# Kernel tuning notes

Measured on AMD Instinct MI355X. Metric: run time of the kernel, lower is better.

## Reference

```python
import jax, jax.numpy as jnp
import numpy as np

NUM_LAYERS = 2
FEATURES = 128
INPUT_SIZE = 128
HIDDEN = 512
BATCH = 128
SEQ_LEN = 512
PRED_LEN = 128


def _uniform(key, shape, fan):
    bound = 1.0 / np.sqrt(fan)
    return jax.random.uniform(key, shape, jnp.float32, -bound, bound)


def setup_inputs() -> dict:
    key = jax.random.key(0)
    ks = jax.random.split(key, 14)
    inp = {}
    inp["x"] = jax.random.normal(ks[0], (BATCH, SEQ_LEN, FEATURES), jnp.float32)
    # encoder Linear(features -> input_size)
    inp["enc_w"] = _uniform(ks[1], (INPUT_SIZE, FEATURES), FEATURES)
    inp["enc_b"] = _uniform(ks[2], (INPUT_SIZE,), FEATURES)
    # decoder Linear(hidden -> input_size)
    inp["dec_w"] = _uniform(ks[3], (INPUT_SIZE, HIDDEN), HIDDEN)
    inp["dec_b"] = _uniform(ks[4], (INPUT_SIZE,), HIDDEN)
    # LSTM layer 0 (input_size -> hidden), gate order i,f,g,o as in PyTorch
    inp["wih0"] = _uniform(ks[5], (4 * HIDDEN, INPUT_SIZE), HIDDEN)
    inp["whh0"] = _uniform(ks[6], (4 * HIDDEN, HIDDEN), HIDDEN)
    inp["bih0"] = _uniform(ks[7], (4 * HIDDEN,), HIDDEN)
    inp["bhh0"] = _uniform(ks[8], (4 * HIDDEN,), HIDDEN)
    # LSTM layer 1 (hidden -> hidden)
    inp["wih1"] = _uniform(ks[9], (4 * HIDDEN, HIDDEN), HIDDEN)
    inp["whh1"] = _uniform(ks[10], (4 * HIDDEN, HIDDEN), HIDDEN)
    inp["bih1"] = _uniform(ks[11], (4 * HIDDEN,), HIDDEN)
    inp["bhh1"] = _uniform(ks[12], (4 * HIDDEN,), HIDDEN)
    inp["pred_len"] = PRED_LEN
    return inp


def _lstm_cell(h, c, inp, wih, whh, bih, bhh):
    g = inp @ wih.T + bih + h @ whh.T + bhh  # [B, 4H]
    i, f, gg, o = jnp.split(g, 4, axis=-1)
    c = jax.nn.sigmoid(f) * c + jax.nn.sigmoid(i) * jnp.tanh(gg)
    h = jax.nn.sigmoid(o) * jnp.tanh(c)
    return h, c


def reference(x, enc_w, enc_b, dec_w, dec_b, wih0, whh0, bih0, bhh0,
              wih1, whh1, bih1, bhh1, pred_len):
    B, S, Fdim = x.shape
    T = S + pred_len - 1
    # pad x to T steps; beyond S the input comes from the previous output
    x_pad = jnp.concatenate([x, jnp.zeros((B, pred_len - 1, Fdim), x.dtype)], axis=1)
    x_t = jnp.transpose(x_pad, (1, 0, 2))  # [T, B, F]

    def step(carry, xs):
        h0, c0, h1, c1, prev_out = carry
        xt, t = xs
        inp = jnp.where(t < S, xt, prev_out)
        e = inp @ enc_w.T + enc_b                    # encoder
        h0, c0 = _lstm_cell(h0, c0, e, wih0, whh0, bih0, bhh0)
        h1, c1 = _lstm_cell(h1, c1, h0, wih1, whh1, bih1, bhh1)
        out = h1 @ dec_w.T + dec_b                   # decoder
        return (h0, c0, h1, c1, out), out

    z = jnp.zeros((B, HIDDEN), x.dtype)
    init = (z, z, z, z, jnp.zeros((B, Fdim), x.dtype))
    _, outs = jax.lax.scan(step, init, (x_t, jnp.arange(T)))
    # keep steps idx >= S-1 (pred_len outputs), back to [B, pred_len, input_size]
    return jnp.transpose(outs[S - 1:], (1, 0, 2))
```

## Files before the change

kernel.cpp:

```cpp
#include <hip/hip_runtime.h>
#include <math.h>

#define HID 512
#define FEAT 128
#define SEQL 512
#define PREDL 128
#define NWG 256
#define R0 648
#define R1 520

__device__ __forceinline__ float sigf_(float x) { return 1.0f / (1.0f + __expf(-x)); }
__device__ __forceinline__ float tanh_(float x) {
  float ax = fabsf(x);
  float e2 = __expf(-2.0f * ax);
  return copysignf((1.0f - e2) / (1.0f + e2), x);
}
__device__ __forceinline__ void stg_sc(float* p, float v) {
  __hip_atomic_store(p, v, __ATOMIC_RELAXED, __HIP_MEMORY_SCOPE_AGENT);
}

__device__ __forceinline__ void bar_arr(int* __restrict__ bar, int grp,
                                        int slot, int phase, int tid) {
  __syncthreads();
  if (tid == 0)
    __hip_atomic_store(bar + grp * 8 + slot, phase, __ATOMIC_RELAXED,
                       __HIP_MEMORY_SCOPE_AGENT);
  asm volatile("" ::: "memory");
}
__device__ __forceinline__ void bar_wai(int* __restrict__ bar, int grp,
                                        int phase, int tid,
                                        int* __restrict__ ldsph) {
  asm volatile("" ::: "memory");
  if (tid < 64) {
    for (;;) {
      int v = phase;
      if (tid < 8)
        v = __hip_atomic_load(bar + grp * 8 + tid, __ATOMIC_RELAXED,
                              __HIP_MEMORY_SCOPE_AGENT);
      if (__ballot(v >= phase) == 0xFFFFFFFFFFFFFFFFULL) break;
      __builtin_amdgcn_s_sleep(1);
    }
    if (tid == 0)
      __hip_atomic_store(ldsph, phase, __ATOMIC_RELAXED,
                         __HIP_MEMORY_SCOPE_WORKGROUP);
  } else {
    float z = 1.0f;
    while (__hip_atomic_load(ldsph, __ATOMIC_RELAXED,
                             __HIP_MEMORY_SCOPE_WORKGROUP) < phase) {
#pragma unroll
      for (int i = 0; i < 64; ++i) z = __builtin_fmaf(z, 1.0000001f, 1.0e-9f);
      asm volatile("" : "+v"(z));
    }
  }
  __syncthreads();
}

__device__ __forceinline__ void load1(const float4* p, float4& r) {
  asm volatile("global_load_dwordx4 %0, %1, off sc0 sc1\n\ts_waitcnt vmcnt(0)"
               : "=&v"(r) : "v"(p) : "memory");
}
__device__ __forceinline__ void issue1(const float4* p, float4& r) {
  asm volatile("global_load_dwordx4 %0, %1, off sc0 sc1"
               : "=&v"(r) : "v"(p) : "memory");
}

__global__ __launch_bounds__(1024, 1) void k_teacher(
    const float* __restrict__ x, const float* __restrict__ ENCW,
    const float* __restrict__ enc_b,
    const float* __restrict__ W0T, const float* __restrict__ W1F,
    const float* __restrict__ bih0, const float* __restrict__ bhh0,
    const float* __restrict__ bih1, const float* __restrict__ bhh1,
    float* __restrict__ h0A, float* __restrict__ h0B,
    float* __restrict__ h1A, float* __restrict__ h1B,
    float* __restrict__ cbuf, int* __restrict__ bar) {
  __shared__ float h0l[4 * R0];
  __shared__ float h1l[4 * R0];
  __shared__ float xl[4 * 132];
  __shared__ float sg0[1024];
  __shared__ float sg1[1024];
  __shared__ int lds_ph;

  const int wg = blockIdx.x, tid = threadIdx.x;
  const int grp = wg >> 3, slot = wg & 7;
  const int b = tid & 3, ul = (tid >> 2) & 63, g = tid >> 8;
  const int n = g * 512 + slot * 64 + ul;
  const int rowoff = n;

  float* h0b[2] = {h0A, h0B};
  float* h1b[2] = {h1A, h1B};
  const float4* W0 = (const float4*)W0T + rowoff;
  const float4* W1 = (const float4*)W1F + rowoff;
  const float4* E4 = (const float4*)ENCW;

  const float bt0 = bih0[n] + bhh0[n];
  const float b1f = bih1[n] + bhh1[n];

  const int ldh0 = (tid < 512);
  const int lu = tid & 511;
  const int fe = (tid >> 2) & 127, be = tid & 3;
  const float encb = enc_b[fe];

  const float* h0row = h0l + b * R0;
  const float* h1row = h1l + b * R0;

  float c_reg = 0.0f;
  int ph = 0;
  if (tid == 0) lds_ph = 0;
  if (tid < 128) {
    const int bx = tid >> 5, f4 = tid & 31;
    *(float4*)(xl + bx * 132 + f4 * 4) =
        *(const float4*)(x + ((size_t)(grp * 4 + bx) * SEQL + 0) * FEAT + f4 * 4);
  }
  __syncthreads();

  for (int t = 0; t < SEQL; ++t) {
    const float* src = (ldh0 ? h0b[(t + 1) & 1] : h1b[t & 1]) + grp * 2048;
    const float4* sp = (const float4*)src + lu;
    float4 r;
    issue1(sp, r);

    if (tid < 512) {
      float e = encb;
#pragma unroll 8
      for (int k4 = 0; k4 < 32; ++k4) {
        const float4 w = E4[k4 * 128 + fe];
        const float4 xv = *(const float4*)(xl + be * 132 + k4 * 4);
        e += w.x * xv.x + w.y * xv.y + w.z * xv.z + w.w * xv.w;
      }
      h0l[be * R0 + 512 + fe] = e;
    }
    asm volatile("s_waitcnt vmcnt(0)" ::: "memory");
    float* dl = ldh0 ? h0l : h1l;
    dl[0 * R0 + lu] = r.x; dl[1 * R0 + lu] = r.y;
    dl[2 * R0 + lu] = r.z; dl[3 * R0 + lu] = r.w;
    __syncthreads();

    float a0 = bt0, a0b = 0.f;
#pragma unroll 4
    for (int k4 = 0; k4 < 160; ++k4) {
      const float4 w = W0[(size_t)k4 * 2048];
      const float4 h = *(const float4*)(h0row + k4 * 4);
      a0 = __builtin_fmaf(w.x, h.x, a0);
      a0b = __builtin_fmaf(w.y, h.y, a0b);
      a0 = __builtin_fmaf(w.z, h.z, a0);
      a0b = __builtin_fmaf(w.w, h.w, a0b);
    }
    a0 += a0b;
    float a1 = b1f, a1b = 0.f;
#pragma unroll 4
    for (int k4 = 0; k4 < 128; ++k4) {
      const float4 w = W1[(size_t)k4 * 2048];
      const float4 h = *(const float4*)(h0row + k4 * 4);
      a1 = __builtin_fmaf(w.x, h.x, a1);
      a1b = __builtin_fmaf(w.y, h.y, a1b);
      a1 = __builtin_fmaf(w.z, h.z, a1);
      a1b = __builtin_fmaf(w.w, h.w, a1b);
    }
#pragma unroll 4
    for (int k4 = 0; k4 < 128; ++k4) {
      const float4 w = W1[(size_t)(128 + k4) * 2048];
      const float4 h = *(const float4*)(h1row + k4 * 4);
      a1 = __builtin_fmaf(w.x, h.x, a1);
      a1b = __builtin_fmaf(w.y, h.y, a1b);
      a1 = __builtin_fmaf(w.z, h.z, a1);
      a1b = __builtin_fmaf(w.w, h.w, a1b);
    }
    a1 += a1b;
    sg0[tid] = a0;
    sg1[tid] = a1;
    __syncthreads();

    if (tid < 256) {
      const float ig = sigf_(sg0[tid]), fg = sigf_(sg0[256 + tid]);
      const float gg = tanh_(sg0[512 + tid]), og = sigf_(sg0[768 + tid]);
      const float cn = fg * c_reg + ig * gg;
      c_reg = cn;
      stg_sc(h0b[t & 1] + grp * 2048 + slot * 256 + tid, og * tanh_(cn));
    } else if (tid < 512 && t > 0) {
      const int l = tid - 256;
      const float ig = sigf_(sg1[l]), fg = sigf_(sg1[256 + l]);
      const float gg = tanh_(sg1[512 + l]), og = sigf_(sg1[768 + l]);
      const float cn = fg * c_reg + ig * gg;
      c_reg = cn;
      stg_sc(h1b[(t + 1) & 1] + grp * 2048 + slot * 256 + l, og * tanh_(cn));
    }
    bar_arr(bar, grp, slot, ++ph, tid);
    if (tid < 128 && t + 1 < SEQL) {
      const int bx = tid >> 5, f4 = tid & 31;
      *(float4*)(xl + bx * 132 + f4 * 4) =
          *(const float4*)(x + ((size_t)(grp * 4 + bx) * SEQL + (t + 1)) * FEAT + f4 * 4);
    }
    bar_wai(bar, grp, ph, tid, &lds_ph);
  }

  if (tid < 256) cbuf[(size_t)wg * 256 + tid] = c_reg;
  else if (tid < 512) cbuf[65536 + (size_t)wg * 256 + (tid - 256)] = c_reg;
}

__global__ __launch_bounds__(1024, 1) void k_ar(
    const float* __restrict__ WAF, const float* __restrict__ W1F,
    const float* __restrict__ DECW, const float* __restrict__ dec_b,
    const float* __restrict__ bih0, const float* __restrict__ bhh0,
    const float* __restrict__ bih1, const float* __restrict__ bhh1,
    const float* __restrict__ bcomp,
    float* __restrict__ h0A, float* __restrict__ h0B,
    float* __restrict__ h1A, float* __restrict__ h1B,
    float* __restrict__ cbuf, int* __restrict__ bar,
    float* __restrict__ out) {
  __shared__ float hAl[4 * R1];
  __shared__ float hBl[4 * R1];
  __shared__ float sg0[1024];
  __shared__ float sg1[1024];
  __shared__ float sdec[256];
  __shared__ int lds_ph;

  const int wg = blockIdx.x, tid = threadIdx.x;
  const int grp = wg >> 3, slot = wg & 7;
  const int b = tid & 3, ul = (tid >> 2) & 63, g = tid >> 8;
  const int n = g * 512 + slot * 64 + ul;

  float* h0b[2] = {h0A, h0B};
  float* h1b[2] = {h1A, h1B};
  const float4* WA = (const float4*)WAF + n;
  const float4* W1 = (const float4*)W1F + n;
  const float4* D4 = (const float4*)DECW;

  const float baf = bih0[n] + bhh0[n] + bcomp[n];
  const float b1f = bih1[n] + bhh1[n];

  const int lu = tid & 511;
  const float* hArow = hAl + b * R1;
  const float* hBrow = hBl + b * R1;

  const int d = tid - 512;
  const int dfl = d & 15, dbb = (d >> 4) & 3, dq = (d >> 6) & 3;
  const int fdec = slot * 16 + dfl;
  const float decb = dec_b[fdec & 127];

  float c_reg = 0.0f;
  if (tid < 256) c_reg = cbuf[(size_t)wg * 256 + tid];
  else if (tid < 512) c_reg = cbuf[65536 + (size_t)wg * 256 + (tid - 256)];

  int ph = 0;
  if (tid == 0) lds_ph = 0;
  __syncthreads();

  {
    const float* src = (tid < 512 ? h0b[1] : h1b[0]) + grp * 2048;
    float4 r;
    load1((const float4*)src + lu, r);
    float* dl = (tid < 512) ? hBl : hAl;
    dl[0 * R1 + lu] = r.x; dl[1 * R1 + lu] = r.y;
    dl[2 * R1 + lu] = r.z; dl[3 * R1 + lu] = r.w;
    __syncthreads();
    float a1 = b1f, a1b = 0.f;
#pragma unroll 4
    for (int k4 = 0; k4 < 128; ++k4) {
      const float4 w = W1[(size_t)k4 * 2048];
      const float4 h = *(const float4*)(hBrow + k4 * 4);
      a1 = __builtin_fmaf(w.x, h.x, a1);  a1b = __builtin_fmaf(w.y, h.y, a1b);
      a1 = __builtin_fmaf(w.z, h.z, a1);  a1b = __builtin_fmaf(w.w, h.w, a1b);
    }
#pragma unroll 4
    for (int k4 = 0; k4 < 128; ++k4) {
      const float4 w = W1[(size_t)(128 + k4) * 2048];
      const float4 h = *(const float4*)(hArow + k4 * 4);
      a1 = __builtin_fmaf(w.x, h.x, a1);  a1b = __builtin_fmaf(w.y, h.y, a1b);
      a1 = __builtin_fmaf(w.z, h.z, a1);  a1b = __builtin_fmaf(w.w, h.w, a1b);
    }
    sg1[tid] = a1 + a1b;
    __syncthreads();
    if (tid >= 256 && tid < 512) {
      const int l = tid - 256;
      const float ig = sigf_(sg1[l]), fg = sigf_(sg1[256 + l]);
      const float gg = tanh_(sg1[512 + l]), og = sigf_(sg1[768 + l]);
      const float cn = fg * c_reg + ig * gg;
      c_reg = cn;
      stg_sc(h1b[1] + grp * 2048 + slot * 256 + l, og * tanh_(cn));
    }
    bar_arr(bar, grp, slot, ++ph, tid);
    bar_wai(bar, grp, ph, tid, &lds_ph);
  }

  for (int t = SEQL; t < SEQL + PREDL - 1; ++t) {
    {
      const float* src = (tid < 512 ? h1b[(t + 1) & 1] : h0b[(t + 1) & 1]) + grp * 2048;
      float4 r;
      load1((const float4*)src + lu, r);
      float* dl = (tid < 512) ? hAl : hBl;
      dl[0 * R1 + lu] = r.x; dl[1 * R1 + lu] = r.y;
      dl[2 * R1 + lu] = r.z; dl[3 * R1 + lu] = r.w;
      __syncthreads();
      float aA = baf, aAb = 0.f;
#pragma unroll 4
      for (int k4 = 0; k4 < 128; ++k4) {
        const float4 w = WA[(size_t)k4 * 2048];
        const float4 h = *(const float4*)(hArow + k4 * 4);
        aA = __builtin_fmaf(w.x, h.x, aA);  aAb = __builtin_fmaf(w.y, h.y, aAb);
        aA = __builtin_fmaf(w.z, h.z, aA);  aAb = __builtin_fmaf(w.w, h.w, aAb);
      }
#pragma unroll 4
      for (int k4 = 0; k4 < 128; ++k4) {
        const float4 w = WA[(size_t)(128 + k4) * 2048];
        const float4 h = *(const float4*)(hBrow + k4 * 4);
        aA = __builtin_fmaf(w.x, h.x, aA);  aAb = __builtin_fmaf(w.y, h.y, aAb);
        aA = __builtin_fmaf(w.z, h.z, aA);  aAb = __builtin_fmaf(w.w, h.w, aAb);
      }
      sg0[tid] = aA + aAb;
      if (tid >= 512 && tid < 768) {
        float p = 0.f;
        const float* hr = hAl + dbb * R1;
#pragma unroll 4
        for (int k4 = dq * 32; k4 < dq * 32 + 32; ++k4) {
          const float4 w = D4[k4 * 128 + fdec];
          const float4 h = *(const float4*)(hr + k4 * 4);
          p += w.x * h.x + w.y * h.y + w.z * h.z + w.w * h.w;
        }
        sdec[d] = p;
      }
      __syncthreads();
      if (tid < 256) {
        const float ig = sigf_(sg0[tid]), fg = sigf_(sg0[256 + tid]);
        const float gg = tanh_(sg0[512 + tid]), og = sigf_(sg0[768 + tid]);
        const float cn = fg * c_reg + ig * gg;
        c_reg = cn;
        stg_sc(h0b[t & 1] + grp * 2048 + slot * 256 + tid, og * tanh_(cn));
      }
      if (tid >= 512 && tid < 576) {
        const float s = decb + sdec[d] + sdec[d + 64] + sdec[d + 128] + sdec[d + 192];
        out[((size_t)(grp * 4 + dbb) * PREDL + (t - SEQL)) * FEAT + fdec] = s;
      }
      bar_arr(bar, grp, slot, ++ph, tid);
      bar_wai(bar, grp, ph, tid, &lds_ph);
    }
    {
      if (tid < 512) {
        const float* src = h0b[t & 1] + grp * 2048;
        float4 r;
        load1((const float4*)src + lu, r);
        hBl[0 * R1 + lu] = r.x; hBl[1 * R1 + lu] = r.y;
        hBl[2 * R1 + lu] = r.z; hBl[3 * R1 + lu] = r.w;
      }
      __syncthreads();
      float a1 = b1f, a1b = 0.f;
#pragma unroll 4
      for (int k4 = 0; k4 < 128; ++k4) {
        const float4 w = W1[(size_t)k4 * 2048];
        const float4 h = *(const float4*)(hBrow + k4 * 4);
        a1 = __builtin_fmaf(w.x, h.x, a1);  a1b = __builtin_fmaf(w.y, h.y, a1b);
        a1 = __builtin_fmaf(w.z, h.z, a1);  a1b = __builtin_fmaf(w.w, h.w, a1b);
      }
#pragma unroll 4
      for (int k4 = 0; k4 < 128; ++k4) {
        const float4 w = W1[(size_t)(128 + k4) * 2048];
        const float4 h = *(const float4*)(hArow + k4 * 4);
        a1 = __builtin_fmaf(w.x, h.x, a1);  a1b = __builtin_fmaf(w.y, h.y, a1b);
        a1 = __builtin_fmaf(w.z, h.z, a1);  a1b = __builtin_fmaf(w.w, h.w, a1b);
      }
      sg1[tid] = a1 + a1b;
      __syncthreads();
      if (tid >= 256 && tid < 512) {
        const int l = tid - 256;
        const float ig = sigf_(sg1[l]), fg = sigf_(sg1[256 + l]);
        const float gg = tanh_(sg1[512 + l]), og = sigf_(sg1[768 + l]);
        const float cn = fg * c_reg + ig * gg;
        c_reg = cn;
        stg_sc(h1b[t & 1] + grp * 2048 + slot * 256 + l, og * tanh_(cn));
      }
      bar_arr(bar, grp, slot, ++ph, tid);
      bar_wai(bar, grp, ph, tid, &lds_ph);
    }
  }

  {
    if (tid < 512) {
      const float* src = h1b[0] + grp * 2048;
      float4 r;
      load1((const float4*)src + lu, r);
      hAl[0 * R1 + lu] = r.x; hAl[1 * R1 + lu] = r.y;
      hAl[2 * R1 + lu] = r.z; hAl[3 * R1 + lu] = r.w;
    }
    __syncthreads();
    if (tid >= 512 && tid < 768) {
      float p = 0.f;
      const float* hr = hAl + dbb * R1;
#pragma unroll 4
      for (int k4 = dq * 32; k4 < dq * 32 + 32; ++k4) {
        const float4 w = D4[k4 * 128 + fdec];
        const float4 h = *(const float4*)(hr + k4 * 4);
        p += w.x * h.x + w.y * h.y + w.z * h.z + w.w * h.w;
      }
      sdec[d] = p;
    }
    __syncthreads();
    if (tid >= 512 && tid < 576) {
      const float s = decb + sdec[d] + sdec[d + 64] + sdec[d + 128] + sdec[d + 192];
      out[((size_t)(grp * 4 + dbb) * PREDL + (PREDL - 1)) * FEAT + fdec] = s;
    }
  }
}

__global__ void k_b1(const float* __restrict__ enc_w,
                     const float* __restrict__ dec_w, float* __restrict__ B1) {
  const int idx = blockIdx.x * 256 + threadIdx.x;
  const int j = idx >> 9, m = idx & 511;
  float acc = 0.0f;
  for (int k = 0; k < FEAT; ++k) acc += enc_w[j * FEAT + k] * dec_w[k * HID + m];
  B1[idx] = acc;
}
__global__ void k_te(const float* __restrict__ enc_w,
                     const float* __restrict__ enc_b,
                     const float* __restrict__ dec_b, float* __restrict__ te) {
  const int j = threadIdx.x;
  float acc = enc_b[j];
  for (int k = 0; k < FEAT; ++k) acc += dec_b[k] * enc_w[j * FEAT + k];
  te[j] = acc;
}
__global__ void k_bcomp(const float* __restrict__ wih0,
                        const float* __restrict__ te, float* __restrict__ bc) {
  const int nn = blockIdx.x * 256 + threadIdx.x;
  float acc = 0.0f;
  for (int j = 0; j < FEAT; ++j) acc += wih0[nn * FEAT + j] * te[j];
  bc[nn] = acc;
}
__global__ void k_w0t(const float* __restrict__ whh0,
                      const float* __restrict__ wih0, float* __restrict__ W) {
  const int idx = blockIdx.x * 256 + threadIdx.x;
  const int k4 = idx >> 11, rr = idx & 2047;
  const int k = k4 * 4;
  float4 v;
  if (k < 512) {
    const float* p = whh0 + (size_t)rr * 512 + k;
    v = make_float4(p[0], p[1], p[2], p[3]);
  } else {
    const float* p = wih0 + (size_t)rr * 128 + (k - 512);
    v = make_float4(p[0], p[1], p[2], p[3]);
  }
  ((float4*)W)[idx] = v;
}
__global__ void k_w1f(const float* __restrict__ wih1,
                      const float* __restrict__ whh1, float* __restrict__ W) {
  const int idx = blockIdx.x * 256 + threadIdx.x;
  const int k4 = idx >> 11, rr = idx & 2047;
  const int k = k4 * 4;
  const float* p = (k < 512) ? (wih1 + (size_t)rr * 512 + k)
                             : (whh1 + (size_t)rr * 512 + (k - 512));
  ((float4*)W)[idx] = make_float4(p[0], p[1], p[2], p[3]);
}
__global__ void k_waf(const float* __restrict__ wih0,
                      const float* __restrict__ B1,
                      const float* __restrict__ whh0, float* __restrict__ W) {
  const int idx = blockIdx.x * 256 + threadIdx.x;
  const int k4 = idx >> 11, rr = idx & 2047;
  const int k = k4 * 4;
  float4 v;
  if (k < 512) {
    float s0 = 0, s1 = 0, s2 = 0, s3 = 0;
    const float* wr = wih0 + (size_t)rr * 128;
    for (int j = 0; j < 128; ++j) {
      const float wv = wr[j];
      const float* bp = B1 + (size_t)j * 512 + k;
      s0 += wv * bp[0]; s1 += wv * bp[1]; s2 += wv * bp[2]; s3 += wv * bp[3];
    }
    v = make_float4(s0, s1, s2, s3);
  } else {
    const float* p = whh0 + (size_t)rr * 512 + (k - 512);
    v = make_float4(p[0], p[1], p[2], p[3]);
  }
  ((float4*)W)[idx] = v;
}
__global__ void k_encw(const float* __restrict__ enc_w, float* __restrict__ W) {
  const int idx = blockIdx.x * 256 + threadIdx.x;
  const int k4 = idx >> 7, f = idx & 127;
  const float* p = enc_w + (size_t)f * 128 + k4 * 4;
  ((float4*)W)[idx] = make_float4(p[0], p[1], p[2], p[3]);
}
__global__ void k_decw(const float* __restrict__ dec_w, float* __restrict__ W) {
  const int idx = blockIdx.x * 256 + threadIdx.x;
  const int k4 = idx >> 7, f = idx & 127;
  const float* p = dec_w + (size_t)f * 512 + k4 * 4;
  ((float4*)W)[idx] = make_float4(p[0], p[1], p[2], p[3]);
}

#define WS_H0A 0
#define WS_H0B 65536
#define WS_H1A 131072
#define WS_H1B 196608
#define WS_CBUF 262144
#define WS_BART 393216
#define WS_BARA 397312
#define WS_TE 401408
#define WS_BCOMP 401536
#define WS_B1 403584
#define WS_ENCW 469120
#define WS_DECW 485504
#define WS_W0T 551040
#define WS_W1F 1861760
#define WS_WAF 3958912

extern "C" void kernel_launch(void* const* d_in, const int* in_sizes, int n_in,
                              void* d_out, int out_size, void* d_ws,
                              size_t ws_size, hipStream_t stream) {
  const float* x     = (const float*)d_in[0];
  const float* enc_w = (const float*)d_in[1];
  const float* enc_b = (const float*)d_in[2];
  const float* dec_w = (const float*)d_in[3];
  const float* dec_b = (const float*)d_in[4];
  const float* wih0  = (const float*)d_in[5];
  const float* whh0  = (const float*)d_in[6];
  const float* bih0  = (const float*)d_in[7];
  const float* bhh0  = (const float*)d_in[8];
  const float* wih1  = (const float*)d_in[9];
  const float* whh1  = (const float*)d_in[10];
  const float* bih1  = (const float*)d_in[11];
  const float* bhh1  = (const float*)d_in[12];
  float* out = (float*)d_out;

  float* ws = (float*)d_ws;
  float* h0A = ws + WS_H0A;
  float* h0B = ws + WS_H0B;
  float* h1A = ws + WS_H1A;
  float* h1B = ws + WS_H1B;
  float* cbuf = ws + WS_CBUF;
  int* barT = (int*)(ws + WS_BART);
  int* barA = (int*)(ws + WS_BARA);
  float* te = ws + WS_TE;
  float* bcomp = ws + WS_BCOMP;
  float* B1 = ws + WS_B1;
  float* ENCW = ws + WS_ENCW;
  float* DECW = ws + WS_DECW;
  float* W0T = ws + WS_W0T;
  float* W1F = ws + WS_W1F;
  float* WAF = ws + WS_WAF;

  (void)hipMemsetAsync(ws, 0, (size_t)262144 * sizeof(float), stream);
  (void)hipMemsetAsync(ws + WS_BART, 0, (size_t)8192 * sizeof(float), stream);

  k_b1<<<256, 256, 0, stream>>>(enc_w, dec_w, B1);
  k_te<<<1, 128, 0, stream>>>(enc_w, enc_b, dec_b, te);
  k_bcomp<<<8, 256, 0, stream>>>(wih0, te, bcomp);
  k_w0t<<<1280, 256, 0, stream>>>(whh0, wih0, W0T);
  k_w1f<<<2048, 256, 0, stream>>>(wih1, whh1, W1F);
  k_waf<<<2048, 256, 0, stream>>>(wih0, B1, whh0, WAF);
  k_encw<<<16, 256, 0, stream>>>(enc_w, ENCW);
  k_decw<<<64, 256, 0, stream>>>(dec_w, DECW);

  k_teacher<<<NWG, 1024, 0, stream>>>(
      x, ENCW, enc_b, W0T, W1F, bih0, bhh0, bih1, bhh1,
      h0A, h0B, h1A, h1B, cbuf, barT);

  k_ar<<<NWG, 1024, 0, stream>>>(
      WAF, W1F, DECW, dec_b, bih0, bhh0, bih1, bhh1, bcomp,
      h0A, h0B, h1A, h1B, cbuf, barA, out);
}
```

Before: 37.98 ms.

## Split teacher phase into per-layer producer/consumer workgroups linked by a ring buffer

Replaces the 256-workgroup teacher kernel, which needed an 8-workgroup global barrier every step, with 64 workgroups. Each batch group of 4 gets one workgroup for layer 0 and one for layer 1, each owning all 2048 gate rows, so the recurrent state stays in LDS. Layer 0 publishes h0 into an 8-deep ring in global memory guarded by producer/consumer counters, which lets the two layers run pipelined instead of in lockstep. The cost is far less parallelism: 64 workgroups instead of 256, each thread computing 8 gate rows per step and streaming the whole weight matrix through one CU.

After: 126.0 ms. 232% more time.

```diff
diff --git a/kernel.cpp b/kernel.cpp
--- a/kernel.cpp
+++ b/kernel.cpp
@@ -8,6 +8,7 @@
 #define NWG 256
 #define R0 648
 #define R1 520
+#define RD 8
 
 __device__ __forceinline__ float sigf_(float x) { return 1.0f / (1.0f + __expf(-x)); }
 __device__ __forceinline__ float tanh_(float x) {
@@ -54,147 +55,218 @@
   }
   __syncthreads();
 }
-
 __device__ __forceinline__ void load1(const float4* p, float4& r) {
   asm volatile("global_load_dwordx4 %0, %1, off sc0 sc1\n\ts_waitcnt vmcnt(0)"
                : "=&v"(r) : "v"(p) : "memory");
 }
-__device__ __forceinline__ void issue1(const float4* p, float4& r) {
-  asm volatile("global_load_dwordx4 %0, %1, off sc0 sc1"
-               : "=&v"(r) : "v"(p) : "memory");
-}
-
-__global__ __launch_bounds__(1024, 1) void k_teacher(
+
+__global__ __launch_bounds__(1024, 1) void k_rails(
     const float* __restrict__ x, const float* __restrict__ ENCW,
     const float* __restrict__ enc_b,
     const float* __restrict__ W0T, const float* __restrict__ W1F,
     const float* __restrict__ bih0, const float* __restrict__ bhh0,
     const float* __restrict__ bih1, const float* __restrict__ bhh1,
-    float* __restrict__ h0A, float* __restrict__ h0B,
-    float* __restrict__ h1A, float* __restrict__ h1B,
-    float* __restrict__ cbuf, int* __restrict__ bar) {
+    float* __restrict__ h0fin,
+    float* __restrict__ h1fin,
+    float* __restrict__ ring, int* __restrict__ pctr, int* __restrict__ cctr,
+    float* __restrict__ cbuf) {
   __shared__ float h0l[4 * R0];
-  __shared__ float h1l[4 * R0];
   __shared__ float xl[4 * 132];
-  __shared__ float sg0[1024];
-  __shared__ float sg1[1024];
-  __shared__ int lds_ph;
+  __shared__ float sg[8192];
+  __shared__ float h1l[4 * R1];
+  __shared__ float h0in[4 * R1];
 
   const int wg = blockIdx.x, tid = threadIdx.x;
-  const int grp = wg >> 3, slot = wg & 7;
-  const int b = tid & 3, ul = (tid >> 2) & 63, g = tid >> 8;
-  const int n = g * 512 + slot * 64 + ul;
-  const int rowoff = n;
-
-  float* h0b[2] = {h0A, h0B};
-  float* h1b[2] = {h1A, h1B};
-  const float4* W0 = (const float4*)W0T + rowoff;
-  const float4* W1 = (const float4*)W1F + rowoff;
-  const float4* E4 = (const float4*)ENCW;
-
-  const float bt0 = bih0[n] + bhh0[n];
-  const float b1f = bih1[n] + bhh1[n];
-
-  const int ldh0 = (tid < 512);
-  const int lu = tid & 511;
-  const int fe = (tid >> 2) & 127, be = tid & 3;
-  const float encb = enc_b[fe];
-
-  const float* h0row = h0l + b * R0;
-  const float* h1row = h1l + b * R0;
-
-  float c_reg = 0.0f;
-  int ph = 0;
-  if (tid == 0) lds_ph = 0;
-  if (tid < 128) {
-    const int bx = tid >> 5, f4 = tid & 31;
-    *(float4*)(xl + bx * 132 + f4 * 4) =
-        *(const float4*)(x + ((size_t)(grp * 4 + bx) * SEQL + 0) * FEAT + f4 * 4);
+  const int w = wg & 31;
+  const int role = wg >> 5;
+  const int g = tid >> 8, u8 = (tid >> 2) & 63, b = tid & 3;
+  const int n0 = g * 512 + u8 * 8;
+  const int u1 = tid >> 2, b1 = tid & 3;
+  const int u2 = (tid + 1024) >> 2, b2 = tid & 3;
+
+  if (role == 0) {
+    const float4* W0 = (const float4*)W0T;
+    const float4* E4 = (const float4*)ENCW;
+    float bs[8];
+#pragma unroll
+    for (int j = 0; j < 8; ++j) bs[j] = bih0[n0 + j] + bhh0[n0 + j];
+    const int fe = (tid >> 2) & 127, be = tid & 3;
+    const float encb = enc_b[fe];
+    const float* hr = h0l + b * R0;
+    float* slotbase = ring + (size_t)w * (RD * 2048);
+
+    for (int i = tid; i < 4 * R0; i += 1024) h0l[i] = 0.0f;
+    float cA = 0.0f, cB = 0.0f;
+    __syncthreads();
+
+    for (int t = 0; t < SEQL; ++t) {
+      if (tid < 128) {
+        const int bx = tid >> 5, f4 = tid & 31;
+        *(float4*)(xl + bx * 132 + f4 * 4) =
+            *(const float4*)(x + ((size_t)(w * 4 + bx) * SEQL + t) * FEAT + f4 * 4);
+      }
+      __syncthreads();
+      if (tid < 512) {
+        float e = encb;
+#pragma unroll 8
+        for (int k4 = 0; k4 < 32; ++k4) {
+          const float4 wv = E4[k4 * 128 + fe];
+          const float4 xv = *(const float4*)(xl + be * 132 + k4 * 4);
+          e += wv.x * xv.x + wv.y * xv.y + wv.z * xv.z + wv.w * xv.w;
+        }
+        h0l[be * R0 + 512 + fe] = e;
+      }
+      __syncthreads();
+
+      float acc[8];
+#pragma unroll
+      for (int j = 0; j < 8; ++j) acc[j] = bs[j];
+#pragma unroll 2
+      for (int k4 = 0; k4 < 160; ++k4) {
+        const float4 h = *(const float4*)(hr + k4 * 4);
+        const float4* wp = W0 + (size_t)k4 * 2048 + n0;
+#pragma unroll
+        for (int j = 0; j < 8; ++j) {
+          const float4 wv = wp[j];
+          acc[j] = __builtin_fmaf(wv.x, h.x,
+                   __builtin_fmaf(wv.y, h.y,
+                   __builtin_fmaf(wv.z, h.z,
+                   __builtin_fmaf(wv.w, h.w, acc[j]))));
+        }
+      }
+#pragma unroll
+      for (int j = 0; j < 8; ++j) sg[g * 2048 + (u8 * 8 + j) * 4 + b] = acc[j];
+      __syncthreads();
+
+      if (t >= RD && tid == 0) {
+        while (__hip_atomic_load(cctr + w * 32, __ATOMIC_RELAXED,
+                                 __HIP_MEMORY_SCOPE_AGENT) < t - (RD - 1))
+          __builtin_amdgcn_s_sleep(2);
+      }
+      __syncthreads();
+
+      float* slot = slotbase + (t & (RD - 1)) * 2048;
+      {
+        const int ci = tid;
+        const float ig = sigf_(sg[ci]), fg = sigf_(sg[2048 + ci]);
+        const float gg = tanh_(sg[4096 + ci]), og = sigf_(sg[6144 + ci]);
+        const float cn = fg * cA + ig * gg;
+        cA = cn;
+        const float hn = og * tanh_(cn);
+        h0l[b1 * R0 + u1] = hn;
+        stg_sc(slot + u1 * 4 + b1, hn);
+        if (t == 511) stg_sc(h0fin + w * 2048 + u1 * 4 + b1, hn);
+      }
+      {
+        const int ci = tid + 1024;
+        const float ig = sigf_(sg[ci]), fg = sigf_(sg[2048 + ci]);
+        const float gg = tanh_(sg[4096 + ci]), og = sigf_(sg[6144 + ci]);
+        const float cn = fg * cB + ig * gg;
+        cB = cn;
+        const float hn = og * tanh_(cn);
+        h0l[b2 * R0 + u2] = hn;
+        stg_sc(slot + u2 * 4 + b2, hn);
+        if (t == 511) stg_sc(h0fin + w * 2048 + u2 * 4 + b2, hn);
+      }
+      __syncthreads();
+      if (tid == 0)
+        __hip_atomic_store(pctr + w * 32, t + 1, __ATOMIC_RELAXED,
+                           __HIP_MEMORY_SCOPE_AGENT);
+    }
+    cbuf[(size_t)(w * 8 + (u1 >> 6)) * 256 + (u1 & 63) * 4 + b1] = cA;
+    cbuf[(size_t)(w * 8 + (u2 >> 6)) * 256 + (u2 & 63) * 4 + b2] = cB;
+  } else {
+    const float4* W1 = (const float4*)W1F;
+    float bs[8];
+#pragma unroll
+    for (int j = 0; j < 8; ++j) bs[j] = bih1[n0 + j] + bhh1[n0 + j];
+    const int lu = tid & 511;
+    const float* hr0 = h0in + b * R1;
+    const float* hr1 = h1l + b * R1;
+    const float* slotbase = ring + (size_t)w * (RD * 2048);
+
+    for (int i = tid; i < 4 * R1; i += 1024) h1l[i] = 0.0f;
+    float cA = 0.0f, cB = 0.0f;
+    __syncthreads();
+
+    for (int t = 0; t <= 510; ++t) {
+      if (tid == 0) {
+        while (__hip_atomic_load(pctr + w * 32, __ATOMIC_RELAXED,
+                                 __HIP_MEMORY_SCOPE_AGENT) < t + 1)
+          __builtin_amdgcn_s_sleep(2);
+      }
+      __syncthreads();
+      if (tid < 512) {
+        const float4* sp =
+            (const float4*)(slotbase + (t & (RD - 1)) * 2048) + lu;
+        float4 r;
+        load1(sp, r);
+        h0in[0 * R1 + lu] = r.x; h0in[1 * R1 + lu] = r.y;
+        h0in[2 * R1 + lu] = r.z; h0in[3 * R1 + lu] = r.w;
+      }
+      __syncthreads();
+      if (tid == 0)
+        __hip_atomic_store(cctr + w * 32, t + 1, __ATOMIC_RELAXED,
+                           __HIP_MEMORY_SCOPE_AGENT);
+
+      float acc[8];
+#pragma unroll
+      for (int j = 0; j < 8; ++j) acc[j] = bs[j];
+#pragma unroll 2
+      for (int k4 = 0; k4 < 128; ++k4) {
+        const float4 h = *(const float4*)(hr0 + k4 * 4);
+        const float4* wp = W1 + (size_t)k4 * 2048 + n0;
+#pragma unroll
+        for (int j = 0; j < 8; ++j) {
+          const float4 wv = wp[j];
+          acc[j] = __builtin_fmaf(wv.x, h.x,
+                   __builtin_fmaf(wv.y, h.y,
+                   __builtin_fmaf(wv.z, h.z,
+                   __builtin_fmaf(wv.w, h.w, acc[j]))));
+        }
+      }
+#pragma unroll 2
+      for (int k4 = 0; k4 < 128; ++k4) {
+        const float4 h = *(const float4*)(hr1 + k4 * 4);
+        const float4* wp = W1 + (size_t)(128 + k4) * 2048 + n0;
+#pragma unroll
+        for (int j = 0; j < 8; ++j) {
+          const float4 wv = wp[j];
+          acc[j] = __builtin_fmaf(wv.x, h.x,
+                   __builtin_fmaf(wv.y, h.y,
+                   __builtin_fmaf(wv.z, h.z,
+                   __builtin_fmaf(wv.w, h.w, acc[j]))));
+        }
+      }
+#pragma unroll
+      for (int j = 0; j < 8; ++j) sg[g * 2048 + (u8 * 8 + j) * 4 + b] = acc[j];
+      __syncthreads();
+
+      {
+        const int ci = tid;
+        const float ig = sigf_(sg[ci]), fg = sigf_(sg[2048 + ci]);
+        const float gg = tanh_(sg[4096 + ci]), og = sigf_(sg[6144 + ci]);
+        const float cn = fg * cA + ig * gg;
+        cA = cn;
+        const float hn = og * tanh_(cn);
+        h1l[b1 * R1 + u1] = hn;
+        if (t == 510) stg_sc(h1fin + w * 2048 + u1 * 4 + b1, hn);
+      }
+      {
+        const int ci = tid + 1024;
+        const float ig = sigf_(sg[ci]), fg = sigf_(sg[2048 + ci]);
+        const float gg = tanh_(sg[4096 + ci]), og = sigf_(sg[6144 + ci]);
+        const float cn = fg * cB + ig * gg;
+        cB = cn;
+        const float hn = og * tanh_(cn);
+        h1l[b2 * R1 + u2] = hn;
+        if (t == 510) stg_sc(h1fin + w * 2048 + u2 * 4 + b2, hn);
+      }
+      __syncthreads();
+    }
+    cbuf[65536 + (size_t)(w * 8 + (u1 >> 6)) * 256 + (u1 & 63) * 4 + b1] = cA;
+    cbuf[65536 + (size_t)(w * 8 + (u2 >> 6)) * 256 + (u2 & 63) * 4 + b2] = cB;
   }
-  __syncthreads();
-
-  for (int t = 0; t < SEQL; ++t) {
-    const float* src = (ldh0 ? h0b[(t + 1) & 1] : h1b[t & 1]) + grp * 2048;
-    const float4* sp = (const float4*)src + lu;
-    float4 r;
-    issue1(sp, r);
-
-    if (tid < 512) {
-      float e = encb;
-#pragma unroll 8
-      for (int k4 = 0; k4 < 32; ++k4) {
-        const float4 w = E4[k4 * 128 + fe];
-        const float4 xv = *(const float4*)(xl + be * 132 + k4 * 4);
-        e += w.x * xv.x + w.y * xv.y + w.z * xv.z + w.w * xv.w;
-      }
-      h0l[be * R0 + 512 + fe] = e;
-    }
-    asm volatile("s_waitcnt vmcnt(0)" ::: "memory");
-    float* dl = ldh0 ? h0l : h1l;
-    dl[0 * R0 + lu] = r.x; dl[1 * R0 + lu] = r.y;
-    dl[2 * R0 + lu] = r.z; dl[3 * R0 + lu] = r.w;
-    __syncthreads();
-
-    float a0 = bt0, a0b = 0.f;
-#pragma unroll 4
-    for (int k4 = 0; k4 < 160; ++k4) {
-      const float4 w = W0[(size_t)k4 * 2048];
-      const float4 h = *(const float4*)(h0row + k4 * 4);
-      a0 = __builtin_fmaf(w.x, h.x, a0);
-      a0b = __builtin_fmaf(w.y, h.y, a0b);
-      a0 = __builtin_fmaf(w.z, h.z, a0);
-      a0b = __builtin_fmaf(w.w, h.w, a0b);
-    }
-    a0 += a0b;
-    float a1 = b1f, a1b = 0.f;
-#pragma unroll 4
-    for (int k4 = 0; k4 < 128; ++k4) {
-      const float4 w = W1[(size_t)k4 * 2048];
-      const float4 h = *(const float4*)(h0row + k4 * 4);
-      a1 = __builtin_fmaf(w.x, h.x, a1);
-      a1b = __builtin_fmaf(w.y, h.y, a1b);
-      a1 = __builtin_fmaf(w.z, h.z, a1);
-      a1b = __builtin_fmaf(w.w, h.w, a1b);
-    }
-#pragma unroll 4
-    for (int k4 = 0; k4 < 128; ++k4) {
-      const float4 w = W1[(size_t)(128 + k4) * 2048];
-      const float4 h = *(const float4*)(h1row + k4 * 4);
-      a1 = __builtin_fmaf(w.x, h.x, a1);
-      a1b = __builtin_fmaf(w.y, h.y, a1b);
-      a1 = __builtin_fmaf(w.z, h.z, a1);
-      a1b = __builtin_fmaf(w.w, h.w, a1b);
-    }
-    a1 += a1b;
-    sg0[tid] = a0;
-    sg1[tid] = a1;
-    __syncthreads();
-
-    if (tid < 256) {
-      const float ig = sigf_(sg0[tid]), fg = sigf_(sg0[256 + tid]);
-      const float gg = tanh_(sg0[512 + tid]), og = sigf_(sg0[768 + tid]);
-      const float cn = fg * c_reg + ig * gg;
-      c_reg = cn;
-      stg_sc(h0b[t & 1] + grp * 2048 + slot * 256 + tid, og * tanh_(cn));
-    } else if (tid < 512 && t > 0) {
-      const int l = tid - 256;
-      const float ig = sigf_(sg1[l]), fg = sigf_(sg1[256 + l]);
-      const float gg = tanh_(sg1[512 + l]), og = sigf_(sg1[768 + l]);
-      const float cn = fg * c_reg + ig * gg;
-      c_reg = cn;
-      stg_sc(h1b[(t + 1) & 1] + grp * 2048 + slot * 256 + l, og * tanh_(cn));
-    }
-    bar_arr(bar, grp, slot, ++ph, tid);
-    if (tid < 128 && t + 1 < SEQL) {
-      const int bx = tid >> 5, f4 = tid & 31;
-      *(float4*)(xl + bx * 132 + f4 * 4) =
-          *(const float4*)(x + ((size_t)(grp * 4 + bx) * SEQL + (t + 1)) * FEAT + f4 * 4);
-    }
-    bar_wai(bar, grp, ph, tid, &lds_ph);
-  }
-
-  if (tid < 256) cbuf[(size_t)wg * 256 + tid] = c_reg;
-  else if (tid < 512) cbuf[65536 + (size_t)wg * 256 + (tid - 256)] = c_reg;
 }
 
 __global__ __launch_bounds__(1024, 1) void k_ar(
@@ -497,6 +569,9 @@
 #define WS_W0T 551040
 #define WS_W1F 1861760
 #define WS_WAF 3958912
+#define WS_RING 6056064
+#define WS_PCTR 6580352
+#define WS_CCTR 6581376
 
 extern "C" void kernel_launch(void* const* d_in, const int* in_sizes, int n_in,
                               void* d_out, int out_size, void* d_ws,
@@ -532,9 +607,14 @@
   float* W0T = ws + WS_W0T;
   float* W1F = ws + WS_W1F;
   float* WAF = ws + WS_WAF;
+  float* ring = ws + WS_RING;
+  int* pctr = (int*)(ws + WS_PCTR);
+  int* cctr = (int*)(ws + WS_CCTR);
+  (void)barT;
 
   (void)hipMemsetAsync(ws, 0, (size_t)262144 * sizeof(float), stream);
   (void)hipMemsetAsync(ws + WS_BART, 0, (size_t)8192 * sizeof(float), stream);
+  (void)hipMemsetAsync(ws + WS_PCTR, 0, (size_t)2048 * sizeof(int), stream);
 
   k_b1<<<256, 256, 0, stream>>>(enc_w, dec_w, B1);
   k_te<<<1, 128, 0, stream>>>(enc_w, enc_b, dec_b, te);
@@ -545,9 +625,9 @@
   k_encw<<<16, 256, 0, stream>>>(enc_w, ENCW);
   k_decw<<<64, 256, 0, stream>>>(dec_w, DECW);
 
-  k_teacher<<<NWG, 1024, 0, stream>>>(
+  k_rails<<<64, 1024, 0, stream>>>(
       x, ENCW, enc_b, W0T, W1F, bih0, bhh0, bih1, bhh1,
-      h0A, h0B, h1A, h1B, cbuf, barT);
+      h0B, h1A, ring, pctr, cctr, cbuf);
 
   k_ar<<<NWG, 1024, 0, stream>>>(
       WAF, W1F, DECW, dec_b, bih0, bhh0, bih1, bhh1, bcomp,
```
